# Kernel tuning notes

Measured on AMD Instinct MI355X. Metric: run time of the kernel, lower is better.

## Reference

```python
import jax, jax.numpy as jnp
import numpy as np

B, N, C, H, M, CC = 8, 1024, 1280, 20, 77, 768
FF = 4 * C
AQ_BITS = 8
W_BITS = 8


def fq_sym(x, bits=AQ_BITS):
    # per-tensor symmetric fake quant with straight-through estimator
    qmax = 2.0 ** (bits - 1) - 1.0
    delta = jnp.maximum(jnp.max(jnp.abs(x)), 1e-8) / qmax
    q = jnp.clip(jnp.round(x / delta), -qmax - 1.0, qmax) * delta
    return x + jax.lax.stop_gradient(q - x)


def fq_zero(x, bits=W_BITS):
    # asymmetric, always_zero (zero point = 0): for softmax probs in [0,1]
    levels = 2.0 ** bits - 1.0
    delta = jnp.maximum(jnp.max(x), 1e-8) / levels
    q = jnp.clip(jnp.round(x / delta), 0.0, levels) * delta
    return x + jax.lax.stop_gradient(q - x)


def layer_norm(x, g, b, eps=1e-5):
    mu = jnp.mean(x, axis=-1, keepdims=True)
    var = jnp.var(x, axis=-1, keepdims=True)
    return (x - mu) * jax.lax.rsqrt(var + eps) * g + b


def attention(x, ctx, Wq, Wk, Wv, Wo, bo, heads):
    b, n, c = x.shape
    m = ctx.shape[1]
    dh = c // heads
    q = fq_sym(x @ Wq)
    k = fq_sym(ctx @ Wk)
    v = fq_sym(ctx @ Wv)
    q = q.reshape(b, n, heads, dh).transpose(0, 2, 1, 3)
    k = k.reshape(b, m, heads, dh).transpose(0, 2, 1, 3)
    v = v.reshape(b, m, heads, dh).transpose(0, 2, 1, 3)
    scores = jnp.einsum('bhnd,bhmd->bhnm', q, k) * (dh ** -0.5)
    w = jax.nn.softmax(scores, axis=-1)
    w = fq_zero(w)  # quantized softmax weights (forces explicit prob materialization)
    out = jnp.einsum('bhnm,bhmd->bhnd', w, v)
    out = out.transpose(0, 2, 1, 3).reshape(b, n, c)
    return out @ Wo + bo


def geglu_ff(x, W1, b1, W2, b2):
    h = x @ W1 + b1
    a, g = jnp.split(h, 2, axis=-1)
    return (a * jax.nn.gelu(g)) @ W2 + b2


def setup_inputs() -> dict:
    key = jax.random.key(0)
    ks = jax.random.split(key, 16)
    s = 0.02
    return {
        'x': jax.random.normal(ks[0], (B, N, C), jnp.float32),
        'ctx': jax.random.normal(ks[1], (B, M, CC), jnp.float32),
        'ln1_g': jnp.ones((C,), jnp.float32), 'ln1_b': jnp.zeros((C,), jnp.float32),
        'ln2_g': jnp.ones((C,), jnp.float32), 'ln2_b': jnp.zeros((C,), jnp.float32),
        'ln3_g': jnp.ones((C,), jnp.float32), 'ln3_b': jnp.zeros((C,), jnp.float32),
        'Wq1': jax.random.normal(ks[2], (C, C), jnp.float32) * s,
        'Wk1': jax.random.normal(ks[3], (C, C), jnp.float32) * s,
        'Wv1': jax.random.normal(ks[4], (C, C), jnp.float32) * s,
        'Wo1': jax.random.normal(ks[5], (C, C), jnp.float32) * s,
        'bo1': jnp.zeros((C,), jnp.float32),
        'Wq2': jax.random.normal(ks[6], (C, C), jnp.float32) * s,
        'Wk2': jax.random.normal(ks[7], (CC, C), jnp.float32) * s,
        'Wv2': jax.random.normal(ks[8], (CC, C), jnp.float32) * s,
        'Wo2': jax.random.normal(ks[9], (C, C), jnp.float32) * s,
        'bo2': jnp.zeros((C,), jnp.float32),
        'Wff1': jax.random.normal(ks[10], (C, 2 * FF), jnp.float32) * s,
        'bff1': jnp.zeros((2 * FF,), jnp.float32),
        'Wff2': jax.random.normal(ks[11], (FF, C), jnp.float32) * s,
        'bff2': jnp.zeros((C,), jnp.float32),
        'heads': H,
    }


def reference(x, ctx, ln1_g, ln1_b, ln2_g, ln2_b, ln3_g, ln3_b,
              Wq1, Wk1, Wv1, Wo1, bo1, Wq2, Wk2, Wv2, Wo2, bo2,
              Wff1, bff1, Wff2, bff2, heads):
    h = attention(layer_norm(x, ln1_g, ln1_b), layer_norm(x, ln1_g, ln1_b),
                  Wq1, Wk1, Wv1, Wo1, bo1, heads)
    x = x + h
    h = attention(layer_norm(x, ln2_g, ln2_b), ctx, Wq2, Wk2, Wv2, Wo2, bo2, heads)
    x = x + h
    x = x + geglu_ff(layer_norm(x, ln3_g, ln3_b), Wff1, bff1, Wff2, bff2)
    return x
```

## Files before the change

kernel.cpp:

```cpp
#include <hip/hip_runtime.h>

typedef __attribute__((ext_vector_type(8))) short bf16x8;
typedef __attribute__((ext_vector_type(4))) float f32x4;

#define DEV __device__ __forceinline__
#define MF(A, B, CACC) CACC = __builtin_amdgcn_mfma_f32_16x16x32_bf16(A, B, CACC, 0, 0, 0)

DEV ushort f2b(float f) {
  unsigned u = __float_as_uint(f);
  u += 0x7fffu + ((u >> 16) & 1u);
  return (ushort)(u >> 16);
}
DEV float b2f(ushort u) { return __uint_as_float(((unsigned)u) << 16); }

DEV void gl_lds16(ushort* lds_base, const ushort* gp) {
  __builtin_amdgcn_global_load_lds(
      (__attribute__((address_space(1))) const void*)gp,
      (__attribute__((address_space(3))) void*)lds_base, 16, 0, 0);
}

__global__ void k_zero(unsigned* p, int n) {
  int i = blockIdx.x * blockDim.x + threadIdx.x;
  if (i < n) p[i] = 0u;
}

__global__ __launch_bounds__(256) void k_wt(const float* __restrict__ W,
                                            ushort* __restrict__ WT, int K, int N) {
  __shared__ float T[32][33];
  int k0 = blockIdx.y * 32, n0 = blockIdx.x * 32;
  int tx = threadIdx.x & 31, ty = threadIdx.x >> 5;
  #pragma unroll
  for (int r = ty; r < 32; r += 8) {
    int k = k0 + r, n = n0 + tx;
    T[r][tx] = (k < K && n < N) ? W[(size_t)k * N + n] : 0.f;
  }
  __syncthreads();
  #pragma unroll
  for (int r = ty; r < 32; r += 8) {
    int n = n0 + r, k = k0 + tx;
    if (n < N && k < K) WT[(size_t)n * K + k] = f2b(T[tx][r]);
  }
}

__global__ void k_cvt(const float* __restrict__ in, ushort* __restrict__ out, int n) {
  int i = blockIdx.x * 256 + threadIdx.x;
  if (i < n) out[i] = f2b(in[i]);
}

__global__ __launch_bounds__(256) void k_ln(const float* __restrict__ x,
    const float* __restrict__ g, const float* __restrict__ b,
    ushort* __restrict__ out) {
  const int C = 1280;
  int row = blockIdx.x, tid = threadIdx.x;
  const float* xr = x + (size_t)row * C;
  float v0 = xr[tid], v1 = xr[tid + 256], v2 = xr[tid + 512],
        v3 = xr[tid + 768], v4 = xr[tid + 1024];
  float s = v0 + v1 + v2 + v3 + v4;
  float ss = v0 * v0 + v1 * v1 + v2 * v2 + v3 * v3 + v4 * v4;
  #pragma unroll
  for (int off = 32; off; off >>= 1) {
    s += __shfl_down(s, off);
    ss += __shfl_down(ss, off);
  }
  __shared__ float red[8];
  __shared__ float mu_s, rstd_s;
  int wave = tid >> 6, lane = tid & 63;
  if (lane == 0) { red[wave] = s; red[4 + wave] = ss; }
  __syncthreads();
  if (tid == 0) {
    float S = red[0] + red[1] + red[2] + red[3];
    float SS = red[4] + red[5] + red[6] + red[7];
    float mu = S / C;
    float var = SS / C - mu * mu;
    mu_s = mu;
    rstd_s = rsqrtf(var + 1e-5f);
  }
  __syncthreads();
  float mu = mu_s, rstd = rstd_s;
  size_t o = (size_t)row * C + tid;
  out[o]        = f2b((v0 - mu) * rstd * g[tid]        + b[tid]);
  out[o + 256]  = f2b((v1 - mu) * rstd * g[tid + 256]  + b[tid + 256]);
  out[o + 512]  = f2b((v2 - mu) * rstd * g[tid + 512]  + b[tid + 512]);
  out[o + 768]  = f2b((v3 - mu) * rstd * g[tid + 768]  + b[tid + 768]);
  out[o + 1024] = f2b((v4 - mu) * rstd * g[tid + 1024] + b[tid + 1024]);
}

DEV void st1(float v, int r_, int c_, int ldc, const float* resid,
             float* Cf, ushort* Cb) {
  size_t o = (size_t)r_ * ldc + c_;
  if (resid) v += resid[o];
  if (Cf) Cf[o] = v;
  if (Cb) Cb[o] = f2b(v);
}
DEV float epi4(f32x4 v, int rbase, int c_, int M, int N, int ldc,
               const float* bias, const float* resid, float* Cf, ushort* Cb) {
  float v0 = v.x, v1 = v.y, v2 = v.z, v3 = v.w;
  float am = fmaxf(fmaxf(fabsf(v0), fabsf(v1)), fmaxf(fabsf(v2), fabsf(v3)));
  if (c_ < N) {
    float bb = bias ? bias[c_] : 0.f;
    v0 += bb; v1 += bb; v2 += bb; v3 += bb;
    if (rbase + 0 < M) st1(v0, rbase + 0, c_, ldc, resid, Cf, Cb);
    if (rbase + 1 < M) st1(v1, rbase + 1, c_, ldc, resid, Cf, Cb);
    if (rbase + 2 < M) st1(v2, rbase + 2, c_, ldc, resid, Cf, Cb);
    if (rbase + 3 < M) st1(v3, rbase + 3, c_, ldc, resid, Cf, Cb);
  }
  return am;
}

__global__ __launch_bounds__(256) void k_gemm(
    const ushort* __restrict__ A, int lda,
    const ushort* __restrict__ BT, int ldb,
    float* __restrict__ Cf, ushort* __restrict__ Cb, int ldc,
    const float* __restrict__ bias, const float* __restrict__ resid,
    unsigned* am_slot, int M, int N, int K) {
  __shared__ __align__(16) ushort SAB[8192];
  int tid = threadIdx.x;
  int wave = tid >> 6, lane = tid & 63;
  int q = lane >> 4, mi = lane & 15;
  int wr = (wave >> 1) * 64, wc = (wave & 1) * 64;
  int bm0 = blockIdx.y * 128, bn0 = blockIdx.x * 128;
  f32x4 c00 = {}, c01 = {}, c02 = {}, c03 = {};
  f32x4 c10 = {}, c11 = {}, c12 = {}, c13 = {};
  f32x4 c20 = {}, c21 = {}, c22 = {}, c23 = {};
  f32x4 c30 = {}, c31 = {}, c32 = {}, c33 = {};
  for (int k0 = 0; k0 < K; k0 += 32) {
    __syncthreads();
    #pragma unroll
    for (int t = 0; t < 4; t++) {
      int c = wave * 256 + t * 64 + lane;
      const ushort* gp;
      if (c < 512) {
        int r = c >> 2, kc = (c & 3) << 3;
        int gr = bm0 + r; if (gr >= M) gr = M - 1;
        gp = A + (size_t)gr * lda + k0 + kc;
      } else {
        int c2 = c - 512;
        int r = c2 >> 2, kc = (c2 & 3) << 3;
        int gn = bn0 + r; if (gn >= N) gn = N - 1;
        gp = BT + (size_t)gn * ldb + k0 + kc;
      }
      gl_lds16(&SAB[(wave * 256 + t * 64) * 8], gp);
    }
    __syncthreads();
    const ushort* Ab = &SAB[(wr + mi) * 32 + q * 8];
    const ushort* Bb = &SAB[4096 + (wc + mi) * 32 + q * 8];
    bf16x8 a0 = *(const bf16x8*)(Ab);
    bf16x8 a1 = *(const bf16x8*)(Ab + 512);
    bf16x8 a2 = *(const bf16x8*)(Ab + 1024);
    bf16x8 a3 = *(const bf16x8*)(Ab + 1536);
    bf16x8 b0 = *(const bf16x8*)(Bb);
    bf16x8 b1 = *(const bf16x8*)(Bb + 512);
    bf16x8 b2 = *(const bf16x8*)(Bb + 1024);
    bf16x8 b3 = *(const bf16x8*)(Bb + 1536);
    MF(a0, b0, c00); MF(a0, b1, c01); MF(a0, b2, c02); MF(a0, b3, c03);
    MF(a1, b0, c10); MF(a1, b1, c11); MF(a1, b2, c12); MF(a1, b3, c13);
    MF(a2, b0, c20); MF(a2, b1, c21); MF(a2, b2, c22); MF(a2, b3, c23);
    MF(a3, b0, c30); MF(a3, b1, c31); MF(a3, b2, c32); MF(a3, b3, c33);
  }
  int rb = bm0 + wr + q * 4, cb = bn0 + wc + mi;
  float am = 0.f;
  am = fmaxf(am, epi4(c00, rb +  0, cb +  0, M, N, ldc, bias, resid, Cf, Cb));
  am = fmaxf(am, epi4(c01, rb +  0, cb + 16, M, N, ldc, bias, resid, Cf, Cb));
  am = fmaxf(am, epi4(c02, rb +  0, cb + 32, M, N, ldc, bias, resid, Cf, Cb));
  am = fmaxf(am, epi4(c03, rb +  0, cb + 48, M, N, ldc, bias, resid, Cf, Cb));
  am = fmaxf(am, epi4(c10, rb + 16, cb +  0, M, N, ldc, bias, resid, Cf, Cb));
  am = fmaxf(am, epi4(c11, rb + 16, cb + 16, M, N, ldc, bias, resid, Cf, Cb));
  am = fmaxf(am, epi4(c12, rb + 16, cb + 32, M, N, ldc, bias, resid, Cf, Cb));
  am = fmaxf(am, epi4(c13, rb + 16, cb + 48, M, N, ldc, bias, resid, Cf, Cb));
  am = fmaxf(am, epi4(c20, rb + 32, cb +  0, M, N, ldc, bias, resid, Cf, Cb));
  am = fmaxf(am, epi4(c21, rb + 32, cb + 16, M, N, ldc, bias, resid, Cf, Cb));
  am = fmaxf(am, epi4(c22, rb + 32, cb + 32, M, N, ldc, bias, resid, Cf, Cb));
  am = fmaxf(am, epi4(c23, rb + 32, cb + 48, M, N, ldc, bias, resid, Cf, Cb));
  am = fmaxf(am, epi4(c30, rb + 48, cb +  0, M, N, ldc, bias, resid, Cf, Cb));
  am = fmaxf(am, epi4(c31, rb + 48, cb + 16, M, N, ldc, bias, resid, Cf, Cb));
  am = fmaxf(am, epi4(c32, rb + 48, cb + 32, M, N, ldc, bias, resid, Cf, Cb));
  am = fmaxf(am, epi4(c33, rb + 48, cb + 48, M, N, ldc, bias, resid, Cf, Cb));
  if (am_slot) {
    #pragma unroll
    for (int off = 32; off; off >>= 1) am = fmaxf(am, __shfl_down(am, off));
    if (lane == 0) atomicMax(am_slot, __float_as_uint(am));
  }
}

__global__ void k_quant(const ushort* __restrict__ in, ushort* __restrict__ out,
                        const unsigned* __restrict__ slot, int n) {
  int i = blockIdx.x * 256 + threadIdx.x;
  if (i >= n) return;
  float delta = fmaxf(__uint_as_float(*slot), 1e-8f) * (1.f / 127.f);
  float x = b2f(in[i]);
  float y = fminf(fmaxf(rintf(x / delta), -128.f), 127.f) * delta;
  out[i] = f2b(y);
}

__global__ __launch_bounds__(256) void k_vt(const ushort* __restrict__ vq,
    ushort* __restrict__ vT, int H, int Mr, int Mpad) {
  const int C = 1280;
  __shared__ __align__(16) ushort T[64][72];
  int bh = blockIdx.y, b = bh / H, h = bh % H;
  int m0 = blockIdx.x * 64;
  int tid = threadIdx.x;
  #pragma unroll
  for (int c = tid; c < 512; c += 256) {
    int mm = c >> 3, dc = (c & 7) << 3;
    int m = m0 + mm;
    int4 val = make_int4(0, 0, 0, 0);
    if (m < Mr) val = *(const int4*)(vq + ((size_t)b * Mr + m) * C + h * 64 + dc);
    *(int4*)&T[mm][dc] = val;
  }
  __syncthreads();
  #pragma unroll
  for (int c = tid; c < 512; c += 256) {
    int dd = c >> 3, mc = (c & 7) << 3;
    unsigned w0 = (unsigned)T[mc + 0][dd] | ((unsigned)T[mc + 1][dd] << 16);
    unsigned w1 = (unsigned)T[mc + 2][dd] | ((unsigned)T[mc + 3][dd] << 16);
    unsigned w2 = (unsigned)T[mc + 4][dd] | ((unsigned)T[mc + 5][dd] << 16);
    unsigned w3 = (unsigned)T[mc + 6][dd] | ((unsigned)T[mc + 7][dd] << 16);
    int4 val = make_int4((int)w0, (int)w1, (int)w2, (int)w3);
    *(int4*)(vT + ((size_t)bh * 64 + dd) * Mpad + m0 + mc) = val;
  }
}

__global__ __launch_bounds__(256) void k_attn1(
    const ushort* __restrict__ qq, const ushort* __restrict__ kq,
    float2* __restrict__ rs, unsigned* __restrict__ pmax,
    int H, int N, int Mr, float cs) {
  const int C = 1280;
  __shared__ __align__(16) ushort Qs[64][72];
  __shared__ __align__(16) ushort Ks[64][72];
  int tid = threadIdx.x;
  int wave = tid >> 6, lane = tid & 63;
  int q = lane >> 4, mi = lane & 15;
  int bh = blockIdx.y, b = bh / H, h = bh % H;
  int r0 = blockIdx.x * 64;
  #pragma unroll
  for (int c = tid; c < 512; c += 256) {
    int r = c >> 3, dc = (c & 7) << 3;
    *(int4*)&Qs[r][dc] = *(const int4*)(qq + ((size_t)b * N + r0 + r) * C + h * 64 + dc);
  }
  float m_run = -3.0e38f, z_run = 0.f;
  int nt = (Mr + 63) >> 6;
  for (int mt = 0; mt < nt; mt++) {
    __syncthreads();
    #pragma unroll
    for (int c = tid; c < 512; c += 256) {
      int mm = c >> 3, dc = (c & 7) << 3;
      int m = mt * 64 + mm;
      int4 val = make_int4(0, 0, 0, 0);
      if (m < Mr) val = *(const int4*)(kq + ((size_t)b * Mr + m) * C + h * 64 + dc);
      *(int4*)&Ks[mm][dc] = val;
    }
    __syncthreads();
    f32x4 s0 = {}, s1 = {}, s2 = {}, s3 = {};
    #pragma unroll
    for (int kc = 0; kc < 2; kc++) {
      bf16x8 qv  = *(const bf16x8*)&Qs[wave * 16 + mi][kc * 32 + q * 8];
      bf16x8 k0v = *(const bf16x8*)&Ks[mi][kc * 32 + q * 8];
      bf16x8 k1v = *(const bf16x8*)&Ks[16 + mi][kc * 32 + q * 8];
      bf16x8 k2v = *(const bf16x8*)&Ks[32 + mi][kc * 32 + q * 8];
      bf16x8 k3v = *(const bf16x8*)&Ks[48 + mi][kc * 32 + q * 8];
      MF(k0v, qv, s0); MF(k1v, qv, s1); MF(k2v, qv, s2); MF(k3v, qv, s3);
    }
    int kb = mt * 64 + q * 4;
    float e0  = (kb + 0  < Mr) ? s0.x * cs : -3.0e38f;
    float e1  = (kb + 1  < Mr) ? s0.y * cs : -3.0e38f;
    float e2  = (kb + 2  < Mr) ? s0.z * cs : -3.0e38f;
    float e3  = (kb + 3  < Mr) ? s0.w * cs : -3.0e38f;
    float e4  = (kb + 16 < Mr) ? s1.x * cs : -3.0e38f;
    float e5  = (kb + 17 < Mr) ? s1.y * cs : -3.0e38f;
    float e6  = (kb + 18 < Mr) ? s1.z * cs : -3.0e38f;
    float e7  = (kb + 19 < Mr) ? s1.w * cs : -3.0e38f;
    float e8  = (kb + 32 < Mr) ? s2.x * cs : -3.0e38f;
    float e9  = (kb + 33 < Mr) ? s2.y * cs : -3.0e38f;
    float e10 = (kb + 34 < Mr) ? s2.z * cs : -3.0e38f;
    float e11 = (kb + 35 < Mr) ? s2.w * cs : -3.0e38f;
    float e12 = (kb + 48 < Mr) ? s3.x * cs : -3.0e38f;
    float e13 = (kb + 49 < Mr) ? s3.y * cs : -3.0e38f;
    float e14 = (kb + 50 < Mr) ? s3.z * cs : -3.0e38f;
    float e15 = (kb + 51 < Mr) ? s3.w * cs : -3.0e38f;
    float tm = fmaxf(fmaxf(fmaxf(fmaxf(e0, e1), fmaxf(e2, e3)),
                           fmaxf(fmaxf(e4, e5), fmaxf(e6, e7))),
                     fmaxf(fmaxf(fmaxf(e8, e9), fmaxf(e10, e11)),
                           fmaxf(fmaxf(e12, e13), fmaxf(e14, e15))));
    float mn = fmaxf(m_run, tm);
    float zs = exp2f(e0 - mn)  + exp2f(e1 - mn)  + exp2f(e2 - mn)  + exp2f(e3 - mn)
             + exp2f(e4 - mn)  + exp2f(e5 - mn)  + exp2f(e6 - mn)  + exp2f(e7 - mn)
             + exp2f(e8 - mn)  + exp2f(e9 - mn)  + exp2f(e10 - mn) + exp2f(e11 - mn)
             + exp2f(e12 - mn) + exp2f(e13 - mn) + exp2f(e14 - mn) + exp2f(e15 - mn);
    z_run = z_run * exp2f(m_run - mn) + zs;
    m_run = mn;
  }
  float mo = fmaxf(m_run, __shfl_xor(m_run, 16));
  mo = fmaxf(mo, __shfl_xor(mo, 32));
  float zz = z_run * exp2f(m_run - mo);
  zz += __shfl_xor(zz, 16);
  zz += __shfl_xor(zz, 32);
  if (q == 0) {
    float2 st; st.x = mo; st.y = zz;
    rs[(size_t)bh * N + r0 + wave * 16 + mi] = st;
  }
  float pm = 1.f / zz;
  #pragma unroll
  for (int off = 32; off; off >>= 1) pm = fmaxf(pm, __shfl_down(pm, off));
  if (lane == 0) atomicMax(pmax, __float_as_uint(pm));
}

DEV ushort q8lvl(float s, float cs, float mc) {
  float p = fminf(rintf(exp2f(fmaf(s, cs, -mc))), 255.f);
  return (ushort)(__float_as_uint(p) >> 16);
}

__global__ __launch_bounds__(256) void k_attn2(
    const ushort* __restrict__ qq, const ushort* __restrict__ kq,
    const ushort* __restrict__ vT, const float2* __restrict__ rs,
    const unsigned* __restrict__ pmax, ushort* __restrict__ ao,
    int H, int N, int Mr, int Mpad, float cs) {
  const int C = 1280;
  __shared__ __align__(16) ushort Qs[64][72];
  __shared__ __align__(16) ushort Ks[64][72];
  __shared__ __align__(16) ushort Vs[64][72];
  __shared__ __align__(16) ushort Ps[64][72];
  int tid = threadIdx.x;
  int wave = tid >> 6, lane = tid & 63;
  int q = lane >> 4, mi = lane & 15;
  int bh = blockIdx.y, b = bh / H, h = bh % H;
  int r0 = blockIdx.x * 64;
  #pragma unroll
  for (int c = tid; c < 512; c += 256) {
    int r = c >> 3, dc = (c & 7) << 3;
    *(int4*)&Qs[r][dc] = *(const int4*)(qq + ((size_t)b * N + r0 + r) * C + h * 64 + dc);
  }
  int rbase = wave * 16 + q * 4;
  float delta = fmaxf(__uint_as_float(*pmax), 1e-8f) * (1.f / 255.f);
  float ld = __log2f(delta);
  float2 st0 = rs[(size_t)bh * N + r0 + rbase + 0];
  float2 st1 = rs[(size_t)bh * N + r0 + rbase + 1];
  float2 st2 = rs[(size_t)bh * N + r0 + rbase + 2];
  float2 st3 = rs[(size_t)bh * N + r0 + rbase + 3];
  float mc0 = st0.x + __log2f(st0.y) + ld;
  float mc1 = st1.x + __log2f(st1.y) + ld;
  float mc2 = st2.x + __log2f(st2.y) + ld;
  float mc3 = st3.x + __log2f(st3.y) + ld;
  f32x4 o0 = {}, o1 = {}, o2 = {}, o3 = {};
  int nt = (Mr + 63) >> 6;
  for (int mt = 0; mt < nt; mt++) {
    __syncthreads();
    #pragma unroll
    for (int c = tid; c < 512; c += 256) {
      int mm = c >> 3, dc = (c & 7) << 3;
      int m = mt * 64 + mm;
      int4 val = make_int4(0, 0, 0, 0);
      if (m < Mr) val = *(const int4*)(kq + ((size_t)b * Mr + m) * C + h * 64 + dc);
      *(int4*)&Ks[mm][dc] = val;
      *(int4*)&Vs[mm][dc] = *(const int4*)(vT + ((size_t)bh * 64 + mm) * Mpad + mt * 64 + dc);
    }
    __syncthreads();
    f32x4 s0 = {}, s1 = {}, s2 = {}, s3 = {};
    #pragma unroll
    for (int kc = 0; kc < 2; kc++) {
      bf16x8 aq  = *(const bf16x8*)&Qs[wave * 16 + mi][kc * 32 + q * 8];
      bf16x8 k0v = *(const bf16x8*)&Ks[mi][kc * 32 + q * 8];
      bf16x8 k1v = *(const bf16x8*)&Ks[16 + mi][kc * 32 + q * 8];
      bf16x8 k2v = *(const bf16x8*)&Ks[32 + mi][kc * 32 + q * 8];
      bf16x8 k3v = *(const bf16x8*)&Ks[48 + mi][kc * 32 + q * 8];
      MF(aq, k0v, s0); MF(aq, k1v, s1); MF(aq, k2v, s2); MF(aq, k3v, s3);
    }
    int mlim = Mr - mt * 64;
    bool ok0 = (mi      < mlim);
    bool ok1 = (16 + mi < mlim);
    bool ok2 = (32 + mi < mlim);
    bool ok3 = (48 + mi < mlim);
    Ps[rbase + 0][mi]      = ok0 ? q8lvl(s0.x, cs, mc0) : (ushort)0;
    Ps[rbase + 1][mi]      = ok0 ? q8lvl(s0.y, cs, mc1) : (ushort)0;
    Ps[rbase + 2][mi]      = ok0 ? q8lvl(s0.z, cs, mc2) : (ushort)0;
    Ps[rbase + 3][mi]      = ok0 ? q8lvl(s0.w, cs, mc3) : (ushort)0;
    Ps[rbase + 0][16 + mi] = ok1 ? q8lvl(s1.x, cs, mc0) : (ushort)0;
    Ps[rbase + 1][16 + mi] = ok1 ? q8lvl(s1.y, cs, mc1) : (ushort)0;
    Ps[rbase + 2][16 + mi] = ok1 ? q8lvl(s1.z, cs, mc2) : (ushort)0;
    Ps[rbase + 3][16 + mi] = ok1 ? q8lvl(s1.w, cs, mc3) : (ushort)0;
    Ps[rbase + 0][32 + mi] = ok2 ? q8lvl(s2.x, cs, mc0) : (ushort)0;
    Ps[rbase + 1][32 + mi] = ok2 ? q8lvl(s2.y, cs, mc1) : (ushort)0;
    Ps[rbase + 2][32 + mi] = ok2 ? q8lvl(s2.z, cs, mc2) : (ushort)0;
    Ps[rbase + 3][32 + mi] = ok2 ? q8lvl(s2.w, cs, mc3) : (ushort)0;
    Ps[rbase + 0][48 + mi] = ok3 ? q8lvl(s3.x, cs, mc0) : (ushort)0;
    Ps[rbase + 1][48 + mi] = ok3 ? q8lvl(s3.y, cs, mc1) : (ushort)0;
    Ps[rbase + 2][48 + mi] = ok3 ? q8lvl(s3.z, cs, mc2) : (ushort)0;
    Ps[rbase + 3][48 + mi] = ok3 ? q8lvl(s3.w, cs, mc3) : (ushort)0;
    asm volatile("s_waitcnt lgkmcnt(0)" ::: "memory");
    __builtin_amdgcn_sched_barrier(0);
    #pragma unroll
    for (int kc = 0; kc < 2; kc++) {
      bf16x8 ap = *(const bf16x8*)&Ps[wave * 16 + mi][kc * 32 + q * 8];
      bf16x8 v0 = *(const bf16x8*)&Vs[mi][kc * 32 + q * 8];
      bf16x8 v1 = *(const bf16x8*)&Vs[16 + mi][kc * 32 + q * 8];
      bf16x8 v2 = *(const bf16x8*)&Vs[32 + mi][kc * 32 + q * 8];
      bf16x8 v3 = *(const bf16x8*)&Vs[48 + mi][kc * 32 + q * 8];
      MF(ap, v0, o0); MF(ap, v1, o1); MF(ap, v2, o2); MF(ap, v3, o3);
    }
  }
  int rr = r0 + wave * 16 + q * 4;
  size_t base = ((size_t)b * N + rr) * C + h * 64 + mi;
  ao[base]              = f2b(o0.x * delta); ao[base + C]          = f2b(o0.y * delta);
  ao[base + 2 * C]      = f2b(o0.z * delta); ao[base + 3 * C]      = f2b(o0.w * delta);
  ao[base + 16]         = f2b(o1.x * delta); ao[base + C + 16]     = f2b(o1.y * delta);
  ao[base + 2 * C + 16] = f2b(o1.z * delta); ao[base + 3 * C + 16] = f2b(o1.w * delta);
  ao[base + 32]         = f2b(o2.x * delta); ao[base + C + 32]     = f2b(o2.y * delta);
  ao[base + 2 * C + 32] = f2b(o2.z * delta); ao[base + 3 * C + 32] = f2b(o2.w * delta);
  ao[base + 48]         = f2b(o3.x * delta); ao[base + C + 48]     = f2b(o3.y * delta);
  ao[base + 2 * C + 48] = f2b(o3.z * delta); ao[base + 3 * C + 48] = f2b(o3.w * delta);
}

#define BAR __builtin_amdgcn_s_barrier()
#define LGKM0 do { asm volatile("s_waitcnt lgkmcnt(0)" ::: "memory"); \
                   __builtin_amdgcn_sched_barrier(0); } while (0)
#define VM6 asm volatile("s_waitcnt vmcnt(6)" ::: "memory")
#define PRIO1 __builtin_amdgcn_s_setprio(1)
#define PRIO0 __builtin_amdgcn_s_setprio(0)

#define RDA01(P) do { \
  fa00 = *(const bf16x8*)&(P)[c0];        fa01 = *(const bf16x8*)&(P)[c1]; \
  fa10 = *(const bf16x8*)&(P)[1024 + c0]; fa11 = *(const bf16x8*)&(P)[1024 + c1]; } while (0)
#define RDA23(P) do { \
  fa20 = *(const bf16x8*)&(P)[2048 + c0]; fa21 = *(const bf16x8*)&(P)[2048 + c1]; \
  fa30 = *(const bf16x8*)&(P)[3072 + c0]; fa31 = *(const bf16x8*)&(P)[3072 + c1]; } while (0)
#define RDB(P, H) do { \
  b00 = *(const bf16x8*)&(P)[(H) + c0];        b01 = *(const bf16x8*)&(P)[(H) + c1]; \
  b10 = *(const bf16x8*)&(P)[(H) + 1024 + c0]; b11 = *(const bf16x8*)&(P)[(H) + 1024 + c1]; \
  b20 = *(const bf16x8*)&(P)[(H) + 2048 + c0]; b21 = *(const bf16x8*)&(P)[(H) + 2048 + c1]; \
  b30 = *(const bf16x8*)&(P)[(H) + 3072 + c0]; b31 = *(const bf16x8*)&(P)[(H) + 3072 + c1]; } while (0)

#define MM8(AX0, AX1, AY0, AY1, C0, C1, C2, C3, D0, D1, D2, D3) \
  MF(AX0, b00, C0); MF(AX1, b01, C0); MF(AX0, b10, C1); MF(AX1, b11, C1); \
  MF(AX0, b20, C2); MF(AX1, b21, C2); MF(AX0, b30, C3); MF(AX1, b31, C3); \
  MF(AY0, b00, D0); MF(AY1, b01, D0); MF(AY0, b10, D1); MF(AY1, b11, D1); \
  MF(AY0, b20, D2); MF(AY1, b21, D2); MF(AY0, b30, D3); MF(AY1, b31, D3)

DEV ushort ggel(float a, float g) {
  float u = 1.5957691216057308f * g * (1.f + 0.044715f * g * g);
  float s = 1.f / (1.f + __expf(-u));
  return f2b(a * g * s);
}
DEV void epi4g(f32x4 va, f32x4 vg, size_t base, float ba, float bg,
               ushort* __restrict__ GG) {
  GG[base]         = ggel(va.x + ba, vg.x + bg);
  GG[base + 5120]  = ggel(va.y + ba, vg.y + bg);
  GG[base + 10240] = ggel(va.z + ba, vg.z + bg);
  GG[base + 15360] = ggel(va.w + ba, vg.w + bg);
}
#define EPIN(nn, P0, Q0, P1, Q1, P2, Q2, P3, Q3) do { \
  int cg = colBase + nn * 16 + mi; \
  float ba = bias[cg], bg = bias[5120 + cg]; \
  size_t b0_ = (size_t)rowBase * 5120 + cg; \
  epi4g(P0, Q0, b0_,             ba, bg, GG); \
  epi4g(P1, Q1, b0_ + 16 * 5120, ba, bg, GG); \
  epi4g(P2, Q2, b0_ + 32 * 5120, ba, bg, GG); \
  epi4g(P3, Q3, b0_ + 48 * 5120, ba, bg, GG); \
} while (0)

__global__ __launch_bounds__(512) void k_ff1_8p(
    const ushort* __restrict__ A,
    const ushort* __restrict__ BT,
    const float* __restrict__ bias,
    ushort* __restrict__ GG) {
  __shared__ __align__(16) ushort SAB[65536];
  int tid = threadIdx.x;
  int wave = tid >> 6, lane = tid & 63;
  int q = lane >> 4, mi = lane & 15;
  int wm = wave >> 1, wn = wave & 1;
  int lr = lane >> 3;
  int lc = ((lane & 7) ^ lr) * 8;

  int wg = blockIdx.x;
  int swz = (wg & 7) * 160 + (wg >> 3);
  int bm0 = (swz & 31) * 256, bn0 = (swz >> 5) * 128;

  const int swzr = (mi & 7) * 8;
  int c0 = (q * 8) ^ swzr, c1 = (32 + q * 8) ^ swzr;
  const ushort* A0p = &SAB[(wm * 64 + mi) * 64];
  const ushort* B0p = &SAB[16384 + (wn * 64 + mi) * 64];
  const ushort* A1p = A0p + 32768;
  const ushort* B1p = B0p + 32768;

  const ushort* gA  = A  + (size_t)(bm0 + wave * 8 + lr) * 1280 + lc;
  const ushort* gBa = BT + (size_t)(bn0 + wave * 8 + lr) * 1280 + lc;
  const ushort* gBg = BT + (size_t)(5120 + bn0 + wave * 8 + lr) * 1280 + lc;
  ushort* lA = &SAB[wave * 512];
  ushort* lB = &SAB[16384 + wave * 512];

  auto stA = [&](int bb, int kt, int call) {
    gl_lds16(lA + bb * 32768 + call * 4096,
             gA + (size_t)call * 81920 + (size_t)kt * 64);
  };
  auto stBa = [&](int bb, int kt, int call) {
    gl_lds16(lB + bb * 32768 + call * 4096,
             gBa + (size_t)call * 81920 + (size_t)kt * 64);
  };
  auto stBg = [&](int bb, int kt, int call) {
    gl_lds16(lB + bb * 32768 + (call + 2) * 4096,
             gBg + (size_t)call * 81920 + (size_t)kt * 64);
  };

  f32x4 cA00 = {}, cA01 = {}, cA02 = {}, cA03 = {};
  f32x4 cA10 = {}, cA11 = {}, cA12 = {}, cA13 = {};
  f32x4 cA20 = {}, cA21 = {}, cA22 = {}, cA23 = {};
  f32x4 cA30 = {}, cA31 = {}, cA32 = {}, cA33 = {};
  f32x4 cG00 = {}, cG01 = {}, cG02 = {}, cG03 = {};
  f32x4 cG10 = {}, cG11 = {}, cG12 = {}, cG13 = {};
  f32x4 cG20 = {}, cG21 = {}, cG22 = {}, cG23 = {};
  f32x4 cG30 = {}, cG31 = {}, cG32 = {}, cG33 = {};
  bf16x8 fa00, fa01, fa10, fa11, fa20, fa21, fa30, fa31;
  bf16x8 b00, b01, b10, b11, b20, b21, b30, b31;

  stBa(0, 0, 0); stBa(0, 0, 1); stBg(0, 0, 0); stBg(0, 0, 1);
  stA(0, 0, 0); stA(0, 0, 1); stA(0, 0, 2); stA(0, 0, 3);
  stBa(1, 1, 0); stBa(1, 1, 1);
  stA(1, 1, 0); stA(1, 1, 1); stA(1, 1, 2); stA(1, 1, 3);
  VM6; BAR;

  for (int it = 0; it < 10; ++it) {
    int t1 = 2 * it + 1;
    int s0 = t1 + 1; if (s0 > 19) s0 = 19;
    int s1 = t1 + 2; if (s1 > 19) s1 = 19;
    RDA01(A0p); RDB(B0p, 0);
    stBg(1, t1, 0); stBg(1, t1, 1);
    BAR; LGKM0;
    PRIO1; MM8(fa00, fa01, fa10, fa11, cA00, cA01, cA02, cA03,
               cA10, cA11, cA12, cA13); PRIO0;
    BAR;
    RDA23(A0p);
    stBa(0, s0, 0); stBa(0, s0, 1);
    BAR; LGKM0;
    PRIO1; MM8(fa20, fa21, fa30, fa31, cA20, cA21, cA22, cA23,
               cA30, cA31, cA32, cA33); PRIO0;
    BAR;
    RDB(B0p, 8192);
    stA(0, s0, 0); stA(0, s0, 1);
    BAR; LGKM0;
    PRIO1; MM8(fa00, fa01, fa10, fa11, cG00, cG01, cG02, cG03,
               cG10, cG11, cG12, cG13); PRIO0;
    BAR;
    stA(0, s0, 2); stA(0, s0, 3);
    BAR;
    PRIO1; MM8(fa20, fa21, fa30, fa31, cG20, cG21, cG22, cG23,
               cG30, cG31, cG32, cG33); PRIO0;
    VM6; BAR;
    RDA01(A1p); RDB(B1p, 0);
    stBg(0, s0, 0); stBg(0, s0, 1);
    BAR; LGKM0;
    PRIO1; MM8(fa00, fa01, fa10, fa11, cA00, cA01, cA02, cA03,
               cA10, cA11, cA12, cA13); PRIO0;
    BAR;
    RDA23(A1p);
    stBa(1, s1, 0); stBa(1, s1, 1);
    BAR; LGKM0;
    PRIO1; MM8(fa20, fa21, fa30, fa31, cA20, cA21, cA22, cA23,
               cA30, cA31, cA32, cA33); PRIO0;
    BAR;
    RDB(B1p, 8192);
    stA(1, s1, 0); stA(1, s1, 1);
    BAR; LGKM0;
    PRIO1; MM8(fa00, fa01, fa10, fa11, cG00, cG01, cG02, cG03,
               cG10, cG11, cG12, cG13); PRIO0;
    BAR;
    stA(1, s1, 2); stA(1, s1, 3);
    BAR;
    PRIO1; MM8(fa20, fa21, fa30, fa31, cG20, cG21, cG22, cG23,
               cG30, cG31, cG32, cG33); PRIO0;
    VM6; BAR;
  }

  int colBase = bn0 + wn * 64;
  int rowBase = bm0 + wm * 64 + q * 4;
  EPIN(0, cA00, cG00, cA10, cG10, cA20, cG20, cA30, cG30);
  EPIN(1, cA01, cG01, cA11, cG11, cA21, cG21, cA31, cG31);
  EPIN(2, cA02, cG02, cA12, cG12, cA22, cG22, cA32, cG32);
  EPIN(3, cA03, cG03, cA13, cG13, cA23, cG23, cA33, cG33);
}

extern "C" void kernel_launch(void* const* d_in, const int* in_sizes, int n_in,
                              void* d_out, int out_size, void* d_ws, size_t ws_size,
                              hipStream_t stream) {
  const float* x_in = (const float*)d_in[0];
  const float* ctx  = (const float*)d_in[1];
  const float* ln1g = (const float*)d_in[2];
  const float* ln1b = (const float*)d_in[3];
  const float* ln2g = (const float*)d_in[4];
  const float* ln2b = (const float*)d_in[5];
  const float* ln3g = (const float*)d_in[6];
  const float* ln3b = (const float*)d_in[7];
  const float* Wq1  = (const float*)d_in[8];
  const float* Wk1  = (const float*)d_in[9];
  const float* Wv1  = (const float*)d_in[10];
  const float* Wo1  = (const float*)d_in[11];
  const float* bo1  = (const float*)d_in[12];
  const float* Wq2  = (const float*)d_in[13];
  const float* Wk2  = (const float*)d_in[14];
  const float* Wv2  = (const float*)d_in[15];
  const float* Wo2  = (const float*)d_in[16];
  const float* bo2  = (const float*)d_in[17];
  const float* Wff1 = (const float*)d_in[18];
  const float* bff1 = (const float*)d_in[19];
  const float* Wff2 = (const float*)d_in[20];
  const float* bff2 = (const float*)d_in[21];
  float* out = (float*)d_out;

  const int NR = 8192;
  const int C = 1280, H = 20, Nseq = 1024, CC = 768;
  const int MR2 = 616;
  const float CS = 0.18033688011112042f;

  char* ws = (char*)d_ws;
  size_t off = 0;
  auto alloc = [&](size_t bytes) -> void* {
    void* p = ws + off;
    off += (bytes + 255) & ~(size_t)255;
    return p;
  };
  unsigned* scal = (unsigned*)alloc(64);
  ushort* Wq1T  = (ushort*)alloc((size_t)C * C * 2);
  ushort* Wk1T  = (ushort*)alloc((size_t)C * C * 2);
  ushort* Wv1T  = (ushort*)alloc((size_t)C * C * 2);
  ushort* Wo1T  = (ushort*)alloc((size_t)C * C * 2);
  ushort* Wq2T  = (ushort*)alloc((size_t)C * C * 2);
  ushort* Wk2T  = (ushort*)alloc((size_t)C * CC * 2);
  ushort* Wv2T  = (ushort*)alloc((size_t)C * CC * 2);
  ushort* Wo2T  = (ushort*)alloc((size_t)C * C * 2);
  ushort* WF1T  = (ushort*)alloc((size_t)10240 * C * 2);
  ushort* WF2T  = (ushort*)alloc((size_t)C * 5120 * 2);
  ushort* LN    = (ushort*)alloc((size_t)NR * C * 2);
  size_t regionR = off;
  ushort* QQ    = (ushort*)alloc((size_t)NR * C * 2);
  ushort* KQ    = (ushort*)alloc((size_t)NR * C * 2);
  ushort* VQ    = (ushort*)alloc((size_t)NR * C * 2);
  ushort* VT    = (ushort*)alloc((size_t)160 * 64 * 1024 * 2);
  float2* RS    = (float2*)alloc((size_t)160 * 1024 * 8);
  ushort* CTXB  = (ushort*)alloc((size_t)MR2 * CC * 2);
  size_t need = off;
  ushort* AO = VQ;
  ushort* GG = (ushort*)(ws + regionR);
  if (ws_size < need) return;

  k_zero<<<1, 64, 0, stream>>>(scal, 8);
  k_wt<<<dim3(40, 40), 256, 0, stream>>>(Wq1, Wq1T, C, C);
  k_wt<<<dim3(40, 40), 256, 0, stream>>>(Wk1, Wk1T, C, C);
  k_wt<<<dim3(40, 40), 256, 0, stream>>>(Wv1, Wv1T, C, C);
  k_wt<<<dim3(40, 40), 256, 0, stream>>>(Wo1, Wo1T, C, C);
  k_wt<<<dim3(40, 40), 256, 0, stream>>>(Wq2, Wq2T, C, C);
  k_wt<<<dim3(40, 24), 256, 0, stream>>>(Wk2, Wk2T, CC, C);
  k_wt<<<dim3(40, 24), 256, 0, stream>>>(Wv2, Wv2T, CC, C);
  k_wt<<<dim3(40, 40), 256, 0, stream>>>(Wo2, Wo2T, C, C);
  k_wt<<<dim3(320, 40), 256, 0, stream>>>(Wff1, WF1T, C, 10240);
  k_wt<<<dim3(40, 160), 256, 0, stream>>>(Wff2, WF2T, 5120, C);

  k_ln<<<NR, 256, 0, stream>>>(x_in, ln1g, ln1b, LN);
  k_gemm<<<dim3(10, 64), 256, 0, stream>>>(LN, C, Wq1T, C, nullptr, QQ, C,
                                           nullptr, nullptr, scal + 0, NR, C, C);
  k_quant<<<(NR * C + 255) / 256, 256, 0, stream>>>(QQ, QQ, scal + 0, NR * C);
  k_gemm<<<dim3(10, 64), 256, 0, stream>>>(LN, C, Wk1T, C, nullptr, KQ, C,
                                           nullptr, nullptr, scal + 1, NR, C, C);
  k_quant<<<(NR * C + 255) / 256, 256, 0, stream>>>(KQ, KQ, scal + 1, NR * C);
  k_gemm<<<dim3(10, 64), 256, 0, stream>>>(LN, C, Wv1T, C, nullptr, VQ, C,
                                           nullptr, nullptr, scal + 2, NR, C, C);
  k_quant<<<(NR * C + 255) / 256, 256, 0, stream>>>(VQ, VQ, scal + 2, NR * C);
  k_vt<<<dim3(16, 160), 256, 0, stream>>>(VQ, VT, H, 1024, 1024);
  k_attn1<<<dim3(16, 160), 256, 0, stream>>>(QQ, KQ, RS, scal + 3, H, Nseq, 1024, CS);
  k_attn2<<<dim3(16, 160), 256, 0, stream>>>(QQ, KQ, VT, RS, scal + 3, AO,
                                             H, Nseq, 1024, 1024, CS);
  k_gemm<<<dim3(10, 64), 256, 0, stream>>>(AO, C, Wo1T, C, out, nullptr, C,
                                           bo1, x_in, nullptr, NR, C, C);

  k_ln<<<NR, 256, 0, stream>>>(out, ln2g, ln2b, LN);
  k_gemm<<<dim3(10, 64), 256, 0, stream>>>(LN, C, Wq2T, C, nullptr, QQ, C,
                                           nullptr, nullptr, scal + 4, NR, C, C);
  k_quant<<<(NR * C + 255) / 256, 256, 0, stream>>>(QQ, QQ, scal + 4, NR * C);
  k_cvt<<<(MR2 * CC + 255) / 256, 256, 0, stream>>>(ctx, CTXB, MR2 * CC);
  k_gemm<<<dim3(10, 5), 256, 0, stream>>>(CTXB, CC, Wk2T, CC, nullptr, KQ, C,
                                          nullptr, nullptr, scal + 5, MR2, C, CC);
  k_quant<<<(MR2 * C + 255) / 256, 256, 0, stream>>>(KQ, KQ, scal + 5, MR2 * C);
  k_gemm<<<dim3(10, 5), 256, 0, stream>>>(CTXB, CC, Wv2T, CC, nullptr, VQ, C,
                                          nullptr, nullptr, scal + 6, MR2, C, CC);
  k_quant<<<(MR2 * C + 255) / 256, 256, 0, stream>>>(VQ, VQ, scal + 6, MR2 * C);
  k_vt<<<dim3(2, 160), 256, 0, stream>>>(VQ, VT, H, 77, 128);
  k_attn1<<<dim3(16, 160), 256, 0, stream>>>(QQ, KQ, RS, scal + 7, H, Nseq, 77, CS);
  k_attn2<<<dim3(16, 160), 256, 0, stream>>>(QQ, KQ, VT, RS, scal + 7, AO,
                                             H, Nseq, 77, 128, CS);
  k_gemm<<<dim3(10, 64), 256, 0, stream>>>(AO, C, Wo2T, C, out, nullptr, C,
                                           bo2, out, nullptr, NR, C, C);

  k_ln<<<NR, 256, 0, stream>>>(out, ln3g, ln3b, LN);
  k_ff1_8p<<<dim3(1280), 512, 0, stream>>>(LN, WF1T, bff1, GG);
  k_gemm<<<dim3(10, 64), 256, 0, stream>>>(GG, 5120, WF2T, 5120, out, nullptr, C,
                                           bff2, out, nullptr, NR, C, 5120);
}
```

Measured before the change: 1.789 ms.

## Add 8-wave 256x128 triple-buffered GEMM kernel for the square projections

Introduces k_gemm8, a 512-thread GEMM with 256x128 output tiles, a triple-buffered LDS pipeline fed by direct global-to-LDS loads, and an XCD-aware block swizzle. It replaces the old 10x64-grid k_gemm for the Q/K/V, output projections and the second FF GEMM. The larger tiles aim for more operand reuse and better overlap of loads with MFMA work. In exchange it uses a large LDS footprint (~144KB), which limits occupancy, and it leaves only 320 workgroups, so tail and wave-fill effects may matter. The tile loop assumes K is a multiple of 64 and that the tile count fits the unroll by three.

New measurement: 1.742 ms. 2.6% less time.

```diff
diff --git a/kernel.cpp b/kernel.cpp
--- a/kernel.cpp
+++ b/kernel.cpp
@@ -413,6 +413,7 @@
 #define LGKM0 do { asm volatile("s_waitcnt lgkmcnt(0)" ::: "memory"); \
                    __builtin_amdgcn_sched_barrier(0); } while (0)
 #define VM6 asm volatile("s_waitcnt vmcnt(6)" ::: "memory")
+#define VM0 asm volatile("s_waitcnt vmcnt(0)" ::: "memory")
 #define PRIO1 __builtin_amdgcn_s_setprio(1)
 #define PRIO0 __builtin_amdgcn_s_setprio(0)
 
@@ -427,12 +428,124 @@
   b10 = *(const bf16x8*)&(P)[(H) + 1024 + c0]; b11 = *(const bf16x8*)&(P)[(H) + 1024 + c1]; \
   b20 = *(const bf16x8*)&(P)[(H) + 2048 + c0]; b21 = *(const bf16x8*)&(P)[(H) + 2048 + c1]; \
   b30 = *(const bf16x8*)&(P)[(H) + 3072 + c0]; b31 = *(const bf16x8*)&(P)[(H) + 3072 + c1]; } while (0)
+#define RDB8(P) RDB(P, 0)
 
 #define MM8(AX0, AX1, AY0, AY1, C0, C1, C2, C3, D0, D1, D2, D3) \
   MF(AX0, b00, C0); MF(AX1, b01, C0); MF(AX0, b10, C1); MF(AX1, b11, C1); \
   MF(AX0, b20, C2); MF(AX1, b21, C2); MF(AX0, b30, C3); MF(AX1, b31, C3); \
   MF(AY0, b00, D0); MF(AY1, b01, D0); MF(AY0, b10, D1); MF(AY1, b11, D1); \
   MF(AY0, b20, D2); MF(AY1, b21, D2); MF(AY0, b30, D3); MF(AY1, b31, D3)
+
+#define GB8(AP, BP, DB, KT) \
+  RDA01(AP); RDB8(BP); \
+  stB(DB, KT, 0); stB(DB, KT, 1); stA(DB, KT, 0); \
+  BAR; LGKM0; \
+  PRIO1; MM8(fa00, fa01, fa10, fa11, c00, c01, c02, c03, c10, c11, c12, c13); PRIO0; \
+  BAR; \
+  RDA23(AP); \
+  stA(DB, KT, 1); stA(DB, KT, 2); stA(DB, KT, 3); \
+  BAR; LGKM0; \
+  PRIO1; MM8(fa20, fa21, fa30, fa31, c20, c21, c22, c23, c30, c31, c32, c33); PRIO0; \
+  VM6; BAR;
+
+#define GT8(AP, BP) \
+  RDA01(AP); RDB8(BP); \
+  BAR; LGKM0; \
+  PRIO1; MM8(fa00, fa01, fa10, fa11, c00, c01, c02, c03, c10, c11, c12, c13); PRIO0; \
+  BAR; \
+  RDA23(AP); \
+  BAR; LGKM0; \
+  PRIO1; MM8(fa20, fa21, fa30, fa31, c20, c21, c22, c23, c30, c31, c32, c33); PRIO0;
+
+__global__ __launch_bounds__(512) void k_gemm8(
+    const ushort* __restrict__ A, int lda,
+    const ushort* __restrict__ BT, int ldb,
+    float* __restrict__ Cf, ushort* __restrict__ Cb, int ldc,
+    const float* __restrict__ bias, const float* __restrict__ resid,
+    unsigned* am_slot, int M, int N, int K) {
+  __shared__ __align__(16) ushort SAB[73728];
+  int tid = threadIdx.x;
+  int wave = tid >> 6, lane = tid & 63;
+  int q = lane >> 4, mi = lane & 15;
+  int wm = wave >> 1, wn = wave & 1;
+  int lr = lane >> 3;
+  int lc = ((lane & 7) ^ lr) * 8;
+
+  int NBN = N >> 7;
+  int nblk = (M >> 8) * NBN;
+  int cpx = nblk >> 3;
+  int wg = blockIdx.x;
+  int swz = (wg & 7) * cpx + (wg >> 3);
+  int bm0 = (swz / NBN) << 8, bn0 = (swz % NBN) << 7;
+
+  const int swzr = (mi & 7) * 8;
+  int c0 = (q * 8) ^ swzr, c1 = (32 + q * 8) ^ swzr;
+  const ushort* A0p = &SAB[(wm * 64 + mi) * 64];
+  const ushort* B0p = &SAB[16384 + (wn * 64 + mi) * 64];
+  const ushort* A1p = A0p + 24576; const ushort* B1p = B0p + 24576;
+  const ushort* A2p = A0p + 49152; const ushort* B2p = B0p + 49152;
+
+  const ushort* gA = A  + (size_t)(bm0 + wave * 8 + lr) * lda + lc;
+  const ushort* gB = BT + (size_t)(bn0 + wave * 8 + lr) * ldb + lc;
+  ushort* lA = &SAB[wave * 512];
+  ushort* lB = &SAB[16384 + wave * 512];
+
+  auto stA = [&](int bb, int kt, int call) {
+    gl_lds16(lA + bb * 24576 + call * 4096,
+             gA + (size_t)call * 64 * lda + (size_t)kt * 64);
+  };
+  auto stB = [&](int bb, int kt, int call) {
+    gl_lds16(lB + bb * 24576 + call * 4096,
+             gB + (size_t)call * 64 * ldb + (size_t)kt * 64);
+  };
+
+  f32x4 c00 = {}, c01 = {}, c02 = {}, c03 = {};
+  f32x4 c10 = {}, c11 = {}, c12 = {}, c13 = {};
+  f32x4 c20 = {}, c21 = {}, c22 = {}, c23 = {};
+  f32x4 c30 = {}, c31 = {}, c32 = {}, c33 = {};
+  bf16x8 fa00, fa01, fa10, fa11, fa20, fa21, fa30, fa31;
+  bf16x8 b00, b01, b10, b11, b20, b21, b30, b31;
+
+  stB(0, 0, 0); stB(0, 0, 1);
+  stA(0, 0, 0); stA(0, 0, 1); stA(0, 0, 2); stA(0, 0, 3);
+  stB(1, 1, 0); stB(1, 1, 1);
+  stA(1, 1, 0); stA(1, 1, 1); stA(1, 1, 2); stA(1, 1, 3);
+  VM6; BAR;
+
+  int NT = K >> 6, NTm = NT - 2;
+  for (int t = 0; t < NTm; t += 3) {
+    GB8(A0p, B0p, 2, t + 2);
+    GB8(A1p, B1p, 0, t + 3);
+    GB8(A2p, B2p, 1, t + 4);
+  }
+  GT8(A0p, B0p);
+  VM0; BAR;
+  GT8(A1p, B1p);
+
+  int rb = bm0 + wm * 64 + q * 4, cb = bn0 + wn * 64 + mi;
+  float am = 0.f;
+  am = fmaxf(am, epi4(c00, rb +  0, cb +  0, M, N, ldc, bias, resid, Cf, Cb));
+  am = fmaxf(am, epi4(c01, rb +  0, cb + 16, M, N, ldc, bias, resid, Cf, Cb));
+  am = fmaxf(am, epi4(c02, rb +  0, cb + 32, M, N, ldc, bias, resid, Cf, Cb));
+  am = fmaxf(am, epi4(c03, rb +  0, cb + 48, M, N, ldc, bias, resid, Cf, Cb));
+  am = fmaxf(am, epi4(c10, rb + 16, cb +  0, M, N, ldc, bias, resid, Cf, Cb));
+  am = fmaxf(am, epi4(c11, rb + 16, cb + 16, M, N, ldc, bias, resid, Cf, Cb));
+  am = fmaxf(am, epi4(c12, rb + 16, cb + 32, M, N, ldc, bias, resid, Cf, Cb));
+  am = fmaxf(am, epi4(c13, rb + 16, cb + 48, M, N, ldc, bias, resid, Cf, Cb));
+  am = fmaxf(am, epi4(c20, rb + 32, cb +  0, M, N, ldc, bias, resid, Cf, Cb));
+  am = fmaxf(am, epi4(c21, rb + 32, cb + 16, M, N, ldc, bias, resid, Cf, Cb));
+  am = fmaxf(am, epi4(c22, rb + 32, cb + 32, M, N, ldc, bias, resid, Cf, Cb));
+  am = fmaxf(am, epi4(c23, rb + 32, cb + 48, M, N, ldc, bias, resid, Cf, Cb));
+  am = fmaxf(am, epi4(c30, rb + 48, cb +  0, M, N, ldc, bias, resid, Cf, Cb));
+  am = fmaxf(am, epi4(c31, rb + 48, cb + 16, M, N, ldc, bias, resid, Cf, Cb));
+  am = fmaxf(am, epi4(c32, rb + 48, cb + 32, M, N, ldc, bias, resid, Cf, Cb));
+  am = fmaxf(am, epi4(c33, rb + 48, cb + 48, M, N, ldc, bias, resid, Cf, Cb));
+  if (am_slot) {
+    #pragma unroll
+    for (int off = 32; off; off >>= 1) am = fmaxf(am, __shfl_down(am, off));
+    if (lane == 0) atomicMax(am_slot, __float_as_uint(am));
+  }
+}
 
 DEV ushort ggel(float a, float g) {
   float u = 1.5957691216057308f * g * (1.f + 0.044715f * g * g);
@@ -652,25 +765,25 @@
   k_wt<<<dim3(40, 160), 256, 0, stream>>>(Wff2, WF2T, 5120, C);
 
   k_ln<<<NR, 256, 0, stream>>>(x_in, ln1g, ln1b, LN);
-  k_gemm<<<dim3(10, 64), 256, 0, stream>>>(LN, C, Wq1T, C, nullptr, QQ, C,
-                                           nullptr, nullptr, scal + 0, NR, C, C);
+  k_gemm8<<<dim3(320), 512, 0, stream>>>(LN, C, Wq1T, C, nullptr, QQ, C,
+                                         nullptr, nullptr, scal + 0, NR, C, C);
   k_quant<<<(NR * C + 255) / 256, 256, 0, stream>>>(QQ, QQ, scal + 0, NR * C);
-  k_gemm<<<dim3(10, 64), 256, 0, stream>>>(LN, C, Wk1T, C, nullptr, KQ, C,
-                                           nullptr, nullptr, scal + 1, NR, C, C);
+  k_gemm8<<<dim3(320), 512, 0, stream>>>(LN, C, Wk1T, C, nullptr, KQ, C,
+                                         nullptr, nullptr, scal + 1, NR, C, C);
   k_quant<<<(NR * C + 255) / 256, 256, 0, stream>>>(KQ, KQ, scal + 1, NR * C);
-  k_gemm<<<dim3(10, 64), 256, 0, stream>>>(LN, C, Wv1T, C, nullptr, VQ, C,
-                                           nullptr, nullptr, scal + 2, NR, C, C);
+  k_gemm8<<<dim3(320), 512, 0, stream>>>(LN, C, Wv1T, C, nullptr, VQ, C,
+                                         nullptr, nullptr, scal + 2, NR, C, C);
   k_quant<<<(NR * C + 255) / 256, 256, 0, stream>>>(VQ, VQ, scal + 2, NR * C);
   k_vt<<<dim3(16, 160), 256, 0, stream>>>(VQ, VT, H, 1024, 1024);
   k_attn1<<<dim3(16, 160), 256, 0, stream>>>(QQ, KQ, RS, scal + 3, H, Nseq, 1024, CS);
   k_attn2<<<dim3(16, 160), 256, 0, stream>>>(QQ, KQ, VT, RS, scal + 3, AO,
                                              H, Nseq, 1024, 1024, CS);
-  k_gemm<<<dim3(10, 64), 256, 0, stream>>>(AO, C, Wo1T, C, out, nullptr, C,
-                                           bo1, x_in, nullptr, NR, C, C);
+  k_gemm8<<<dim3(320), 512, 0, stream>>>(AO, C, Wo1T, C, out, nullptr, C,
+                                         bo1, x_in, nullptr, NR, C, C);
 
   k_ln<<<NR, 256, 0, stream>>>(out, ln2g, ln2b, LN);
-  k_gemm<<<dim3(10, 64), 256, 0, stream>>>(LN, C, Wq2T, C, nullptr, QQ, C,
-                                           nullptr, nullptr, scal + 4, NR, C, C);
+  k_gemm8<<<dim3(320), 512, 0, stream>>>(LN, C, Wq2T, C, nullptr, QQ, C,
+                                         nullptr, nullptr, scal + 4, NR, C, C);
   k_quant<<<(NR * C + 255) / 256, 256, 0, stream>>>(QQ, QQ, scal + 4, NR * C);
   k_cvt<<<(MR2 * CC + 255) / 256, 256, 0, stream>>>(ctx, CTXB, MR2 * CC);
   k_gemm<<<dim3(10, 5), 256, 0, stream>>>(CTXB, CC, Wk2T, CC, nullptr, KQ, C,
@@ -683,11 +796,11 @@
   k_attn1<<<dim3(16, 160), 256, 0, stream>>>(QQ, KQ, RS, scal + 7, H, Nseq, 77, CS);
   k_attn2<<<dim3(16, 160), 256, 0, stream>>>(QQ, KQ, VT, RS, scal + 7, AO,
                                              H, Nseq, 77, 128, CS);
-  k_gemm<<<dim3(10, 64), 256, 0, stream>>>(AO, C, Wo2T, C, out, nullptr, C,
-                                           bo2, out, nullptr, NR, C, C);
+  k_gemm8<<<dim3(320), 512, 0, stream>>>(AO, C, Wo2T, C, out, nullptr, C,
+                                         bo2, out, nullptr, NR, C, C);
 
   k_ln<<<NR, 256, 0, stream>>>(out, ln3g, ln3b, LN);
   k_ff1_8p<<<dim3(1280), 512, 0, stream>>>(LN, WF1T, bff1, GG);
-  k_gemm<<<dim3(10, 64), 256, 0, stream>>>(GG, 5120, WF2T, 5120, out, nullptr, C,
-                                           bff2, out, nullptr, NR, C, 5120);
-}
+  k_gemm8<<<dim3(320), 512, 0, stream>>>(GG, 5120, WF2T, 5120, out, nullptr, C,
+                                         bff2, out, nullptr, NR, C, 5120);
+}
```
